# Optimization experiments

Measured on AMD Instinct MI355X. Metric: run time of the kernel, lower is better.

Reference implementation:

```python
import jax, jax.numpy as jnp
import numpy as np

# AlphaPose skeleton (directed, as used by the module) -------------------
_EDGES = [(0,5),(0,6),(1,2),(2,4),(1,3),(5,7),(7,9),(6,8),(8,10),(5,6),
          (5,11),(6,12),(11,12),(11,13),(13,15),(12,14),(14,16)]
_N = 17

def _gcn_norm_adj():
    # PyG GCNConv: add self-loops, deg from target (col), norm = d^-1/2[src]*d^-1/2[dst]
    A = np.zeros((_N, _N), dtype=np.float32)
    for s, t in _EDGES:
        A[t, s] = 1.0               # message flows source -> target
    A += np.eye(_N, dtype=np.float32)  # self loops
    deg = A.sum(axis=1)                # in-degree incl. self loop
    dinv = 1.0 / np.sqrt(deg)
    return (dinv[:, None] * A * dinv[None, :]).astype(np.float32)

A_HAT = jnp.asarray(_gcn_norm_adj())  # [17,17], A_hat[t,s]

B, T, F, H, LH, C = 256, 128, 2, 128, 256, 1


def setup_inputs() -> dict:
    key = jax.random.key(0)
    ks = jax.random.split(key, 8)
    s = 0.05
    return {
        "keypoints": jax.random.normal(ks[0], (B, T, _N, F), jnp.float32),
        "W1": jax.random.normal(ks[1], (F, H), jnp.float32) * s,
        "b1": jnp.zeros((H,), jnp.float32),
        "W2": jax.random.normal(ks[2], (H, H), jnp.float32) * s,
        "b2": jnp.zeros((H,), jnp.float32),
        "W_ih": jax.random.normal(ks[3], (4 * LH, H), jnp.float32) * s,
        "W_hh": jax.random.normal(ks[4], (4 * LH, LH), jnp.float32) * s,
        "b_ih": jnp.zeros((4 * LH,), jnp.float32),
        "b_hh": jnp.zeros((4 * LH,), jnp.float32),
        "W_fc": jax.random.normal(ks[5], (C, LH), jnp.float32) * s,
        "b_fc": jnp.zeros((C,), jnp.float32),
    }


def _lstm(x, W_ih, W_hh, b_ih, b_hh):
    # x: [B, T, H] -> hs: [B, T, LH]; PyTorch gate order i, f, g, o
    b, lh = x.shape[0], W_hh.shape[1]
    bias = b_ih + b_hh
    xw = jnp.einsum('bth,gh->btg', x, W_ih) + bias  # precompute input proj

    def step(carry, xt):
        h, c = carry
        z = xt + h @ W_hh.T
        i, f, g, o = jnp.split(z, 4, axis=-1)
        i, f, o = jax.nn.sigmoid(i), jax.nn.sigmoid(f), jax.nn.sigmoid(o)
        g = jnp.tanh(g)
        c = f * c + i * g
        h = o * jnp.tanh(c)
        return (h, c), h

    h0 = jnp.zeros((b, lh), x.dtype)
    _, hs = jax.lax.scan(step, (h0, h0), xw.transpose(1, 0, 2))
    return hs.transpose(1, 0, 2)


def reference(keypoints, W1, b1, W2, b2, W_ih, W_hh, b_ih, b_hh, W_fc, b_fc):
    # Batched GCNConv: out = A_hat @ (X W) + b, fused over all B*T frames
    x = jnp.einsum('nm,btmh->btnh', A_HAT, keypoints @ W1) + b1
    x = jax.nn.relu(x)
    x = jnp.einsum('nm,btmh->btnh', A_HAT, x @ W2) + b2
    x = jax.nn.relu(x)
    pooled = x.mean(axis=2)                      # global_mean_pool -> [B,T,H]
    hs = _lstm(pooled, W_ih, W_hh, b_ih, b_hh)   # [B,T,LH]
    feat = hs.max(axis=1)                        # max over time -> [B,LH]
    out = feat @ W_fc.T + b_fc                   # [B,1]
    return jax.nn.sigmoid(out).squeeze(1)        # [B]
```

## Files before the change

kernel.cpp:

```cpp
#include <hip/hip_runtime.h>
#include <hip/hip_bf16.h>
#include <math.h>

#define NNODE 17
#define HF    128
#define TT    128
#define BB    256
#define LHID  256
#define G4    1024

typedef short short8 __attribute__((ext_vector_type(8)));
typedef float f32x4  __attribute__((ext_vector_type(4)));

#define OFF_AHAT   0
#define OFF_WIT    512
#define OFF_BIAS   (OFF_WIT + 131072)
#define OFF_WPK    (OFF_BIAS + 1024)
#define OFF_POOLED (OFF_WPK + 131072)
#define OFF_XW     (OFF_POOLED + 4194304)
#define OFF_FEAT   (OFF_XW + 33554432)

__device__ inline unsigned int f2bf(float x) {
    unsigned int u = __float_as_uint(x);
    return (u + 0x7fffu + ((u >> 16) & 1u)) >> 16;
}

__global__ __launch_bounds__(64) void prep_ahat_k(float* __restrict__ Ahat) {
    __shared__ float A[289];
    __shared__ float dinv[NNODE];
    const int t = threadIdx.x;
    for (int i = t; i < 289; i += 64) A[i] = 0.f;
    __syncthreads();
    if (t == 0) {
        const int es[17] = {0,0,1,2,1,5,7,6,8,5,5,6,11,11,13,12,14};
        const int et[17] = {5,6,2,4,3,7,9,8,10,6,11,12,12,13,15,14,16};
        for (int e = 0; e < 17; e++) A[et[e]*17 + es[e]] = 1.f;
        for (int n = 0; n < NNODE; n++) A[n*17 + n] += 1.f;
    }
    __syncthreads();
    if (t < NNODE) {
        float s = 0.f;
        for (int m = 0; m < NNODE; m++) s += A[t*17 + m];
        dinv[t] = rsqrtf(s);
    }
    __syncthreads();
    for (int i = t; i < 289; i += 64) {
        int n = i / 17, m = i % 17;
        Ahat[i] = dinv[n] * A[i] * dinv[m];
    }
}

__global__ __launch_bounds__(256) void prep_wt_k(
    const float* __restrict__ Wih,
    const float* __restrict__ bih, const float* __restrict__ bhh,
    float* __restrict__ WIT, float* __restrict__ bias_sum)
{
    const int k = blockIdx.x;
    const int g0 = threadIdx.x;
    for (int g = g0; g < G4; g += 256)
        WIT[(size_t)k*G4 + g] = Wih[(size_t)g*HF + k];
    if (k == 0)
        for (int g = g0; g < G4; g += 256)
            bias_sum[g] = bih[g] + bhh[g];
}

__global__ __launch_bounds__(256) void prep_pack_k(
    const float* __restrict__ Whh, unsigned short* __restrict__ Wpk)
{
    const int tid = blockIdx.x * 256 + threadIdx.x;
    const int lane = tid & 63;
    const int kc   = (tid >> 6) & 7;
    const int t    = (tid >> 9) & 7;
    const int w    = (tid >> 12) & 7;
    const int col  = w*128 + t*16 + (lane & 15);
    const int kb   = kc*32 + (lane >> 4)*8;
    const float4 v0 = *(const float4*)(Whh + (size_t)col*LHID + kb);
    const float4 v1 = *(const float4*)(Whh + (size_t)col*LHID + kb + 4);
    uint4 o;
    o.x = f2bf(v0.x) | (f2bf(v0.y) << 16);
    o.y = f2bf(v0.z) | (f2bf(v0.w) << 16);
    o.z = f2bf(v1.x) | (f2bf(v1.y) << 16);
    o.w = f2bf(v1.z) | (f2bf(v1.w) << 16);
    *(uint4*)(Wpk + (size_t)tid*8) = o;
}

__global__ __launch_bounds__(128) void gcn_pool_k(
    const float* __restrict__ kp, const float* __restrict__ W1,
    const float* __restrict__ b1, const float* __restrict__ W2,
    const float* __restrict__ b2, const float* __restrict__ Ahat,
    float* __restrict__ pooled)
{
    const int f = blockIdx.x;
    const int j = threadIdx.x;
    __shared__ float Ah[289];
    __shared__ float X[34];
    __shared__ float AhT[128][20];
    if (j < 34) X[j] = kp[(size_t)f*34 + j];
    for (int i = j; i < 289; i += 128) Ah[i] = Ahat[i];
    __syncthreads();
    float ax0[NNODE], ax1[NNODE];
    #pragma unroll
    for (int n = 0; n < NNODE; n++) {
        float s0 = 0.f, s1 = 0.f;
        #pragma unroll
        for (int m = 0; m < NNODE; m++) {
            float a = Ah[n*17 + m];
            s0 += a * X[2*m];
            s1 += a * X[2*m + 1];
        }
        ax0[n] = s0; ax1[n] = s1;
    }
    const float w10 = W1[j], w11 = W1[HF + j], bb1 = b1[j];
    float h1[NNODE];
    #pragma unroll
    for (int n = 0; n < NNODE; n++)
        h1[n] = fmaxf(fmaf(ax0[n], w10, fmaf(ax1[n], w11, bb1)), 0.f);
    float gcol[NNODE];
    #pragma unroll
    for (int n = 0; n < NNODE; n++) {
        float s = 0.f;
        #pragma unroll
        for (int m = 0; m < NNODE; m++) s += Ah[n*17 + m] * h1[m];
        gcol[n] = s;
    }
    #pragma unroll
    for (int n = 0; n < NNODE; n++) AhT[j][n] = gcol[n];
    __syncthreads();
    float acc[NNODE];
    #pragma unroll
    for (int n = 0; n < NNODE; n++) acc[n] = 0.f;
    for (int k = 0; k < HF; k++) {
        float w = W2[k*HF + j];
        #pragma unroll
        for (int n = 0; n < NNODE; n++) acc[n] = fmaf(AhT[k][n], w, acc[n]);
    }
    const float bb2 = b2[j];
    float s = 0.f;
    #pragma unroll
    for (int n = 0; n < NNODE; n++) s += fmaxf(acc[n] + bb2, 0.f);
    pooled[(size_t)f*HF + j] = s * (1.f/17.f);
}

__global__ __launch_bounds__(256) void xw_gemm_k(
    const float* __restrict__ pooled, const float* __restrict__ WIT,
    const float* __restrict__ bias_sum, float* __restrict__ xw)
{
    const int row0 = blockIdx.x * 16;
    const int col  = blockIdx.y * 256 + threadIdx.x;
    __shared__ float P[16][HF];
    #pragma unroll
    for (int i = 0; i < 8; i++) {
        int e = threadIdx.x + i*256;
        P[e >> 7][e & 127] = pooled[(size_t)(row0 + (e >> 7))*HF + (e & 127)];
    }
    __syncthreads();
    float acc[16];
    #pragma unroll
    for (int r = 0; r < 16; r++) acc[r] = 0.f;
    for (int k = 0; k < HF; k++) {
        float w = WIT[(size_t)k*G4 + col];
        #pragma unroll
        for (int r = 0; r < 16; r++) acc[r] = fmaf(P[r][k], w, acc[r]);
    }
    float bs = bias_sum[col];
    #pragma unroll
    for (int r = 0; r < 16; r++)
        xw[(size_t)(row0 + r)*G4 + col] = acc[r] + bs;
}

__global__ __launch_bounds__(512, 2) void lstm_mfma_k(
    const float* __restrict__ xw, const unsigned short* __restrict__ Wpk,
    float* __restrict__ feat)
{
    const int b0  = blockIdx.x * 8;
    const int tid = threadIdx.x;
    const int w   = tid >> 6;
    const int l   = tid & 63;
    const int eu0 = (tid & 63) << 2;

    __shared__ float zbuf[8][G4];
    __shared__ unsigned short hpack[8][64][8];

    ((uint4*)hpack)[tid] = make_uint4(0u, 0u, 0u, 0u);

    float c[4]  = {0.f, 0.f, 0.f, 0.f};
    float hm[4] = {-1e30f, -1e30f, -1e30f, -1e30f};
    const unsigned short* wbase = Wpk + (size_t)w*32768 + l*8;
    const float* xwrow = xw + ((size_t)(b0 + w)*TT)*G4 + eu0;
    __syncthreads();

    for (int t = 0; t < TT; ++t) {
        float4 xg[4];
        #pragma unroll
        for (int g = 0; g < 4; ++g)
            xg[g] = *(const float4*)(xwrow + (size_t)t*G4 + g*256);

        short8 a[8];
        #pragma unroll
        for (int kc = 0; kc < 8; ++kc)
            a[kc] = *(const short8*)&hpack[kc][l][0];

        short8 bcur[8], bnext[8];
        #pragma unroll
        for (int kc = 0; kc < 8; ++kc)
            bcur[kc] = *(const short8*)(wbase + kc*512);
        for (int tt = 0; tt < 8; ++tt) {
            if (tt < 7) {
                #pragma unroll
                for (int kc = 0; kc < 8; ++kc)
                    bnext[kc] = *(const short8*)(wbase + (tt+1)*4096 + kc*512);
            }
            f32x4 acc = {0.f, 0.f, 0.f, 0.f};
            #pragma unroll
            for (int kc = 0; kc < 8; ++kc)
                acc = __builtin_amdgcn_mfma_f32_16x16x32_bf16(a[kc], bcur[kc], acc, 0, 0, 0);
            if (l < 32) {
                const int zr = (l >> 4) * 4;
                const int zc = w*128 + tt*16 + (l & 15);
                #pragma unroll
                for (int r = 0; r < 4; ++r) zbuf[zr + r][zc] = acc[r];
            }
            #pragma unroll
            for (int kc = 0; kc < 8; ++kc) bcur[kc] = bnext[kc];
        }
        __syncthreads();

        float4 zi = *(const float4*)&zbuf[w][0*256 + eu0];
        float4 zf = *(const float4*)&zbuf[w][1*256 + eu0];
        float4 zg = *(const float4*)&zbuf[w][2*256 + eu0];
        float4 zo = *(const float4*)&zbuf[w][3*256 + eu0];
        float hval[4];
        #pragma unroll
        for (int q = 0; q < 4; ++q) {
            float vi = ((const float*)&zi)[q] + ((const float*)&xg[0])[q];
            float vf = ((const float*)&zf)[q] + ((const float*)&xg[1])[q];
            float vg = ((const float*)&zg)[q] + ((const float*)&xg[2])[q];
            float vo = ((const float*)&zo)[q] + ((const float*)&xg[3])[q];
            float ii = __builtin_amdgcn_rcpf(1.f + __expf(-vi));
            float ff = __builtin_amdgcn_rcpf(1.f + __expf(-vf));
            float gg = 1.f - 2.f * __builtin_amdgcn_rcpf(__expf(2.f*vg) + 1.f);
            float oo = 1.f / (1.f + __expf(-vo));
            float cn = fmaf(ff, c[q], ii * gg);
            c[q] = cn;
            float th = 1.f - 2.f * __builtin_amdgcn_rcpf(__expf(2.f*cn) + 1.f);
            float hh = oo * th;
            hm[q] = fmaxf(hm[q], hh);
            hval[q] = hh;
        }
        unsigned int p01 = f2bf(hval[0]) | (f2bf(hval[1]) << 16);
        unsigned int p23 = f2bf(hval[2]) | (f2bf(hval[3]) << 16);
        *(uint2*)&hpack[eu0 >> 5][((eu0 >> 3) & 3)*16 + w][eu0 & 7] = make_uint2(p01, p23);
        __syncthreads();
    }
    *(float4*)(feat + (size_t)(b0 + w)*LHID + eu0) = make_float4(hm[0], hm[1], hm[2], hm[3]);
}

__global__ __launch_bounds__(64) void final_k(
    const float* __restrict__ feat, const float* __restrict__ Wfc,
    const float* __restrict__ bfc, float* __restrict__ out)
{
    const int b = blockIdx.x * 64 + threadIdx.x;
    float s = bfc[0];
    for (int u = 0; u < LHID; u++)
        s = fmaf(feat[(size_t)b*LHID + u], Wfc[u], s);
    out[b] = 1.f / (1.f + __expf(-s));
}

extern "C" void kernel_launch(void* const* d_in, const int* in_sizes, int n_in,
                              void* d_out, int out_size, void* d_ws, size_t ws_size,
                              hipStream_t stream) {
    const float* kp  = (const float*)d_in[0];
    const float* W1  = (const float*)d_in[1];
    const float* b1  = (const float*)d_in[2];
    const float* W2  = (const float*)d_in[3];
    const float* b2  = (const float*)d_in[4];
    const float* Wih = (const float*)d_in[5];
    const float* Whh = (const float*)d_in[6];
    const float* bih = (const float*)d_in[7];
    const float* bhh = (const float*)d_in[8];
    const float* Wfc = (const float*)d_in[9];
    const float* bfc = (const float*)d_in[10];

    float* ws     = (float*)d_ws;
    float* Ahat   = ws + OFF_AHAT;
    float* WIT    = ws + OFF_WIT;
    float* bias   = ws + OFF_BIAS;
    unsigned short* Wpk = (unsigned short*)(ws + OFF_WPK);
    float* pooled = ws + OFF_POOLED;
    float* xw     = ws + OFF_XW;
    float* feat   = ws + OFF_FEAT;
    float* out    = (float*)d_out;

    hipLaunchKernelGGL(prep_ahat_k, dim3(1), dim3(64), 0, stream, Ahat);
    hipLaunchKernelGGL(prep_wt_k, dim3(128), dim3(256), 0, stream,
                       Wih, bih, bhh, WIT, bias);
    hipLaunchKernelGGL(prep_pack_k, dim3(128), dim3(256), 0, stream, Whh, Wpk);
    hipLaunchKernelGGL(gcn_pool_k, dim3(BB*TT), dim3(128), 0, stream,
                       kp, W1, b1, W2, b2, Ahat, pooled);
    hipLaunchKernelGGL(xw_gemm_k, dim3(BB*TT/16, 4), dim3(256), 0, stream,
                       pooled, WIT, bias, xw);
    hipLaunchKernelGGL(lstm_mfma_k, dim3(BB/8), dim3(512), 0, stream, xw, Wpk, feat);
    hipLaunchKernelGGL(final_k, dim3(4), dim3(64), 0, stream, feat, Wfc, bfc, out);
}
```

Before: 1.501 ms.

## Split LSTM recurrent matmul K dimension across two wave groups per block

Doubles the LSTM block to 1024 threads and splits the K=256 hidden reduction into two halves, so each wave does 4 MFMAs per tile instead of 8. The partial sums go to two padded zbuf slices and are added in the gate stage, where each thread now handles 2 hidden units instead of 4. The intent is to shorten the per-timestep serial critical path in the latency-bound recurrence. It doubles LDS for zbuf and adds reduction reads, and the grid stays at 32 blocks, so overall CU usage is still low.

```diff
diff --git a/kernel.cpp b/kernel.cpp
--- a/kernel.cpp
+++ b/kernel.cpp
@@ -8,6 +8,7 @@
 #define BB    256
 #define LHID  256
 #define G4    1024
+#define ZSTR  1032
 
 typedef short short8 __attribute__((ext_vector_type(8)));
 typedef float f32x4  __attribute__((ext_vector_type(4)));
@@ -168,7 +169,7 @@
         xw[(size_t)(row0 + r)*G4 + col] = acc[r] + bs;
 }
 
-__global__ __launch_bounds__(512, 2) void lstm_mfma_k(
+__global__ __launch_bounds__(1024, 4) void lstm_mfma_k(
     const float* __restrict__ xw, const unsigned short* __restrict__ Wpk,
     float* __restrict__ feat)
 {
@@ -176,83 +177,91 @@
     const int tid = threadIdx.x;
     const int w   = tid >> 6;
     const int l   = tid & 63;
-    const int eu0 = (tid & 63) << 2;
-
-    __shared__ float zbuf[8][G4];
+    const int kh  = w >> 3;
+    const int cg  = w & 7;
+    const int row = tid >> 7;
+    const int u0  = (tid & 127) * 2;
+
+    __shared__ float zbuf[2][8][ZSTR];
     __shared__ unsigned short hpack[8][64][8];
 
-    ((uint4*)hpack)[tid] = make_uint4(0u, 0u, 0u, 0u);
-
-    float c[4]  = {0.f, 0.f, 0.f, 0.f};
-    float hm[4] = {-1e30f, -1e30f, -1e30f, -1e30f};
-    const unsigned short* wbase = Wpk + (size_t)w*32768 + l*8;
-    const float* xwrow = xw + ((size_t)(b0 + w)*TT)*G4 + eu0;
+    if (tid < 512) ((uint4*)hpack)[tid] = make_uint4(0u, 0u, 0u, 0u);
+
+    float c0 = 0.f, c1 = 0.f;
+    float hm0 = -1e30f, hm1 = -1e30f;
+    const unsigned short* wb = Wpk + (size_t)cg*32768 + (size_t)kh*2048 + (size_t)l*8;
+    const float* xb = xw + ((size_t)(b0 + row)*TT)*G4 + u0;
+    const int zr = (l >> 4) * 4;
+    const int zc = cg*128 + (l & 15);
     __syncthreads();
 
     for (int t = 0; t < TT; ++t) {
-        float4 xg[4];
+        float2 xg[4];
         #pragma unroll
         for (int g = 0; g < 4; ++g)
-            xg[g] = *(const float4*)(xwrow + (size_t)t*G4 + g*256);
-
-        short8 a[8];
-        #pragma unroll
-        for (int kc = 0; kc < 8; ++kc)
-            a[kc] = *(const short8*)&hpack[kc][l][0];
-
-        short8 bcur[8], bnext[8];
-        #pragma unroll
-        for (int kc = 0; kc < 8; ++kc)
-            bcur[kc] = *(const short8*)(wbase + kc*512);
+            xg[g] = *(const float2*)(xb + (size_t)t*G4 + g*256);
+
+        short8 a[4];
+        #pragma unroll
+        for (int kc = 0; kc < 4; ++kc)
+            a[kc] = *(const short8*)&hpack[kh*4 + kc][l][0];
+
+        short8 bc[4], bn[4];
+        #pragma unroll
+        for (int kc = 0; kc < 4; ++kc)
+            bc[kc] = *(const short8*)(wb + kc*512);
         for (int tt = 0; tt < 8; ++tt) {
             if (tt < 7) {
                 #pragma unroll
-                for (int kc = 0; kc < 8; ++kc)
-                    bnext[kc] = *(const short8*)(wbase + (tt+1)*4096 + kc*512);
+                for (int kc = 0; kc < 4; ++kc)
+                    bn[kc] = *(const short8*)(wb + (tt+1)*4096 + kc*512);
             }
             f32x4 acc = {0.f, 0.f, 0.f, 0.f};
             #pragma unroll
-            for (int kc = 0; kc < 8; ++kc)
-                acc = __builtin_amdgcn_mfma_f32_16x16x32_bf16(a[kc], bcur[kc], acc, 0, 0, 0);
+            for (int kc = 0; kc < 4; ++kc)
+                acc = __builtin_amdgcn_mfma_f32_16x16x32_bf16(a[kc], bc[kc], acc, 0, 0, 0);
             if (l < 32) {
-                const int zr = (l >> 4) * 4;
-                const int zc = w*128 + tt*16 + (l & 15);
                 #pragma unroll
-                for (int r = 0; r < 4; ++r) zbuf[zr + r][zc] = acc[r];
+                for (int r = 0; r < 4; ++r)
+                    zbuf[kh][zr + r][tt*16 + zc] = acc[r];
             }
             #pragma unroll
-            for (int kc = 0; kc < 8; ++kc) bcur[kc] = bnext[kc];
+            for (int kc = 0; kc < 4; ++kc) bc[kc] = bn[kc];
         }
         __syncthreads();
 
-        float4 zi = *(const float4*)&zbuf[w][0*256 + eu0];
-        float4 zf = *(const float4*)&zbuf[w][1*256 + eu0];
-        float4 zg = *(const float4*)&zbuf[w][2*256 + eu0];
-        float4 zo = *(const float4*)&zbuf[w][3*256 + eu0];
-        float hval[4];
-        #pragma unroll
-        for (int q = 0; q < 4; ++q) {
-            float vi = ((const float*)&zi)[q] + ((const float*)&xg[0])[q];
-            float vf = ((const float*)&zf)[q] + ((const float*)&xg[1])[q];
-            float vg = ((const float*)&zg)[q] + ((const float*)&xg[2])[q];
-            float vo = ((const float*)&zo)[q] + ((const float*)&xg[3])[q];
+        float2 ziA = *(const float2*)&zbuf[0][row][0*256 + u0];
+        float2 ziB = *(const float2*)&zbuf[1][row][0*256 + u0];
+        float2 zfA = *(const float2*)&zbuf[0][row][1*256 + u0];
+        float2 zfB = *(const float2*)&zbuf[1][row][1*256 + u0];
+        float2 zgA = *(const float2*)&zbuf[0][row][2*256 + u0];
+        float2 zgB = *(const float2*)&zbuf[1][row][2*256 + u0];
+        float2 zoA = *(const float2*)&zbuf[0][row][3*256 + u0];
+        float2 zoB = *(const float2*)&zbuf[1][row][3*256 + u0];
+        float hval[2];
+        #pragma unroll
+        for (int q = 0; q < 2; ++q) {
+            float vi = ((const float*)&ziA)[q] + ((const float*)&ziB)[q] + ((const float*)&xg[0])[q];
+            float vf = ((const float*)&zfA)[q] + ((const float*)&zfB)[q] + ((const float*)&xg[1])[q];
+            float vg = ((const float*)&zgA)[q] + ((const float*)&zgB)[q] + ((const float*)&xg[2])[q];
+            float vo = ((const float*)&zoA)[q] + ((const float*)&zoB)[q] + ((const float*)&xg[3])[q];
             float ii = __builtin_amdgcn_rcpf(1.f + __expf(-vi));
             float ff = __builtin_amdgcn_rcpf(1.f + __expf(-vf));
             float gg = 1.f - 2.f * __builtin_amdgcn_rcpf(__expf(2.f*vg) + 1.f);
             float oo = 1.f / (1.f + __expf(-vo));
-            float cn = fmaf(ff, c[q], ii * gg);
-            c[q] = cn;
+            float cc = (q == 0) ? c0 : c1;
+            float cn = fmaf(ff, cc, ii * gg);
+            if (q == 0) c0 = cn; else c1 = cn;
             float th = 1.f - 2.f * __builtin_amdgcn_rcpf(__expf(2.f*cn) + 1.f);
             float hh = oo * th;
-            hm[q] = fmaxf(hm[q], hh);
+            if (q == 0) hm0 = fmaxf(hm0, hh); else hm1 = fmaxf(hm1, hh);
             hval[q] = hh;
         }
-        unsigned int p01 = f2bf(hval[0]) | (f2bf(hval[1]) << 16);
-        unsigned int p23 = f2bf(hval[2]) | (f2bf(hval[3]) << 16);
-        *(uint2*)&hpack[eu0 >> 5][((eu0 >> 3) & 3)*16 + w][eu0 & 7] = make_uint2(p01, p23);
+        unsigned int hp = f2bf(hval[0]) | (f2bf(hval[1]) << 16);
+        *(unsigned int*)&hpack[u0 >> 5][((u0 >> 3) & 3)*16 + row][u0 & 7] = hp;
         __syncthreads();
     }
-    *(float4*)(feat + (size_t)(b0 + w)*LHID + eu0) = make_float4(hm[0], hm[1], hm[2], hm[3]);
+    *(float2*)(feat + (size_t)(b0 + row)*LHID + u0) = make_float2(hm0, hm1);
 }
 
 __global__ __launch_bounds__(64) void final_k(
@@ -299,6 +308,6 @@
                        kp, W1, b1, W2, b2, Ahat, pooled);
     hipLaunchKernelGGL(xw_gemm_k, dim3(BB*TT/16, 4), dim3(256), 0, stream,
                        pooled, WIT, bias, xw);
-    hipLaunchKernelGGL(lstm_mfma_k, dim3(BB/8), dim3(512), 0, stream, xw, Wpk, feat);
+    hipLaunchKernelGGL(lstm_mfma_k, dim3(BB/8), dim3(1024), 0, stream, xw, Wpk, feat);
     hipLaunchKernelGGL(final_k, dim3(4), dim3(64), 0, stream, feat, Wfc, bfc, out);
 }
```

Result: slower. 1.601 ms (+6.6%).

## Keep LSTM recurrent weights resident in registers and prefetch next-step input projections

Applied to the files above, without the earlier changes.

Each warp's slice of the packed W_hh (64 short8 vectors per lane, 256 VGPRs) is loaded once before the time loop instead of being re-read from global memory on every timestep. The asm barrier keeps the weights in registers. The next timestep's xw gate inputs are also prefetched during the current step's gate math, hiding their global latency. With launch bounds of 512 threads and 2 blocks this risks heavy register pressure, spills or reduced occupancy.

```diff
diff --git a/kernel.cpp b/kernel.cpp
--- a/kernel.cpp
+++ b/kernel.cpp
@@ -176,54 +176,62 @@
     const int tid = threadIdx.x;
     const int w   = tid >> 6;
     const int l   = tid & 63;
-    const int eu0 = (tid & 63) << 2;
+    const int eu0 = l << 2;
 
     __shared__ float zbuf[8][G4];
     __shared__ unsigned short hpack[8][64][8];
 
     ((uint4*)hpack)[tid] = make_uint4(0u, 0u, 0u, 0u);
 
+    const unsigned short* wb = Wpk + (size_t)w*32768 + (size_t)l*8;
+    short8 wreg[8][8];
+    #pragma unroll
+    for (int tt = 0; tt < 8; ++tt) {
+        #pragma unroll
+        for (int kc = 0; kc < 8; ++kc) {
+            wreg[tt][kc] = *(const short8*)(wb + tt*4096 + kc*512);
+            asm volatile("" : "+v"(wreg[tt][kc]));
+        }
+    }
+
     float c[4]  = {0.f, 0.f, 0.f, 0.f};
     float hm[4] = {-1e30f, -1e30f, -1e30f, -1e30f};
-    const unsigned short* wbase = Wpk + (size_t)w*32768 + l*8;
     const float* xwrow = xw + ((size_t)(b0 + w)*TT)*G4 + eu0;
+    const int zr = (l >> 4) * 4;
+    const int zc = w*128 + (l & 15);
+
+    float4 xg[4];
+    #pragma unroll
+    for (int g = 0; g < 4; ++g)
+        xg[g] = *(const float4*)(xwrow + g*256);
     __syncthreads();
 
     for (int t = 0; t < TT; ++t) {
-        float4 xg[4];
-        #pragma unroll
-        for (int g = 0; g < 4; ++g)
-            xg[g] = *(const float4*)(xwrow + (size_t)t*G4 + g*256);
-
         short8 a[8];
         #pragma unroll
         for (int kc = 0; kc < 8; ++kc)
             a[kc] = *(const short8*)&hpack[kc][l][0];
 
-        short8 bcur[8], bnext[8];
-        #pragma unroll
-        for (int kc = 0; kc < 8; ++kc)
-            bcur[kc] = *(const short8*)(wbase + kc*512);
+        #pragma unroll
         for (int tt = 0; tt < 8; ++tt) {
-            if (tt < 7) {
-                #pragma unroll
-                for (int kc = 0; kc < 8; ++kc)
-                    bnext[kc] = *(const short8*)(wbase + (tt+1)*4096 + kc*512);
-            }
             f32x4 acc = {0.f, 0.f, 0.f, 0.f};
             #pragma unroll
             for (int kc = 0; kc < 8; ++kc)
-                acc = __builtin_amdgcn_mfma_f32_16x16x32_bf16(a[kc], bcur[kc], acc, 0, 0, 0);
+                acc = __builtin_amdgcn_mfma_f32_16x16x32_bf16(a[kc], wreg[tt][kc], acc, 0, 0, 0);
             if (l < 32) {
-                const int zr = (l >> 4) * 4;
-                const int zc = w*128 + tt*16 + (l & 15);
                 #pragma unroll
-                for (int r = 0; r < 4; ++r) zbuf[zr + r][zc] = acc[r];
+                for (int r = 0; r < 4; ++r)
+                    zbuf[zr + r][tt*16 + zc] = acc[r];
             }
+        }
+        __syncthreads();
+
+        float4 xgn[4];
+        if (t + 1 < TT) {
             #pragma unroll
-            for (int kc = 0; kc < 8; ++kc) bcur[kc] = bnext[kc];
-        }
-        __syncthreads();
+            for (int g = 0; g < 4; ++g)
+                xgn[g] = *(const float4*)(xwrow + (size_t)(t+1)*G4 + g*256);
+        }
 
         float4 zi = *(const float4*)&zbuf[w][0*256 + eu0];
         float4 zf = *(const float4*)&zbuf[w][1*256 + eu0];
@@ -251,6 +259,9 @@
         unsigned int p23 = f2bf(hval[2]) | (f2bf(hval[3]) << 16);
         *(uint2*)&hpack[eu0 >> 5][((eu0 >> 3) & 3)*16 + w][eu0 & 7] = make_uint2(p01, p23);
         __syncthreads();
+
+        #pragma unroll
+        for (int g = 0; g < 4; ++g) xg[g] = xgn[g];
     }
     *(float4*)(feat + (size_t)(b0 + w)*LHID + eu0) = make_float4(hm[0], hm[1], hm[2], hm[3]);
 }
```

After: 1.597 ms. +6.3%, slower.
